# Kernel optimization log

Hardware: AMD Instinct MI355X
Metric: run time of the kernel (lower is better)

Reference implementation:

```python
import jax, jax.numpy as jnp
import numpy as np

EMBED = 1024
HEADS = 16
HEAD_DIM = EMBED // HEADS


def setup_inputs() -> dict:
    key = jax.random.key(0)
    ks = jax.random.split(key, 8)
    N, S = 4, 2048
    scale = 1.0 / np.sqrt(HEAD_DIM)
    return {
        "values": jax.random.normal(ks[0], (N, S, EMBED), jnp.float32),
        "keys": jax.random.normal(ks[1], (N, S, EMBED), jnp.float32),
        "query": jax.random.normal(ks[2], (N, S, EMBED), jnp.float32),
        "Wv": jax.random.normal(ks[3], (HEAD_DIM, HEAD_DIM), jnp.float32) * scale,
        "Wk": jax.random.normal(ks[4], (HEAD_DIM, HEAD_DIM), jnp.float32) * scale,
        "Wq": jax.random.normal(ks[5], (HEAD_DIM, HEAD_DIM), jnp.float32) * scale,
        "Wo": jax.random.normal(ks[6], (EMBED, EMBED), jnp.float32) / np.sqrt(EMBED),
        "bo": jax.random.normal(ks[7], (EMBED,), jnp.float32) * 0.01,
    }


def reference(values, keys, query, Wv, Wk, Wq, Wo, bo):
    N = query.shape[0]
    # reshape to [N, S, H, D]
    v = values.reshape(N, -1, HEADS, HEAD_DIM)
    k = keys.reshape(N, -1, HEADS, HEAD_DIM)
    q = query.reshape(N, -1, HEADS, HEAD_DIM)
    # per-head linear projections (torch Linear: x @ W.T)
    v = jnp.einsum("nshd,ed->nshe", v, Wv)
    k = jnp.einsum("nshd,ed->nshe", k, Wk)
    q = jnp.einsum("nshd,ed->nshe", q, Wq)
    # full attention matrix [N, H, Q, K]; note scale uses embed_size**0.5 as in source
    energy = jnp.einsum("nqhd,nkhd->nhqk", q, k)
    attn = jax.nn.softmax(energy / jnp.sqrt(jnp.asarray(EMBED, energy.dtype)), axis=3)
    out = jnp.einsum("nhql,nlhd->nqhd", attn, v).reshape(N, -1, EMBED)
    return out @ Wo.T + bo
```

## Files before the change

kernel.cpp:

```cpp
#include <hip/hip_runtime.h>
#include <hip/hip_bf16.h>

#define EMBED 1024
#define HEADS 16
#define HD    64
#define NB    4
#define SEQ   2048

typedef __bf16 bf16x8 __attribute__((ext_vector_type(8)));
typedef float  f32x4  __attribute__((ext_vector_type(4)));

__device__ __forceinline__ unsigned short f2bf(float f) {
    union { float f; unsigned u; } v; v.f = f;
    unsigned r = v.u + 0x7fffu + ((v.u >> 16) & 1u);
    return (unsigned short)(r >> 16);
}
__device__ __forceinline__ unsigned pack2(float a, float b) {
    return (unsigned)f2bf(a) | ((unsigned)f2bf(b) << 16);
}

__global__ __launch_bounds__(256) void cvt_kernel(const float* __restrict__ src,
                                                  unsigned short* __restrict__ dst) {
    int i = blockIdx.x * 256 + threadIdx.x;
    float4 v = ((const float4*)src)[i];
    ushort4 o;
    o.x = f2bf(v.x); o.y = f2bf(v.y); o.z = f2bf(v.z); o.w = f2bf(v.w);
    ((ushort4*)dst)[i] = o;
}

__global__ __launch_bounds__(256) void proj_kernel(
    const float* __restrict__ xq, const float* __restrict__ xk, const float* __restrict__ xv,
    const float* __restrict__ Wq, const float* __restrict__ Wk, const float* __restrict__ Wv,
    unsigned short* __restrict__ Qp, unsigned short* __restrict__ Kp, unsigned short* __restrict__ Vt)
{
    __shared__ __align__(16) unsigned short Wl[64 * 72];
    __shared__ __align__(16) unsigned short Xl[256 * 72];

    int bx = blockIdx.x;
    int p  = bx >> 9;
    int r  = bx & 511;
    int st = r & 7, h = (r >> 3) & 15, n = r >> 7;
    int s0 = st * 256;

    const float* x = (p == 0) ? xq : (p == 1) ? xk : xv;
    const float* W = (p == 0) ? Wq : (p == 1) ? Wk : Wv;
    const float sc = (p == 0) ? 0.045084220027780106f : 1.0f;

    int tid = threadIdx.x;

    for (int i = 0; i < 4; ++i) {
        int idx = tid + i * 256;
        int row = idx >> 4, c4 = idx & 15;
        float4 wv = ((const float4*)W)[row * 16 + c4];
        int o = row * 72 + c4 * 4;
        Wl[o] = f2bf(wv.x); Wl[o+1] = f2bf(wv.y); Wl[o+2] = f2bf(wv.z); Wl[o+3] = f2bf(wv.w);
    }
    const float* xbase = x + (size_t)(n * SEQ + s0) * EMBED + h * HD;
    for (int i = 0; i < 16; ++i) {
        int idx = tid + i * 256;
        int row = idx >> 4, c4 = idx & 15;
        float4 v = *(const float4*)(xbase + (size_t)row * EMBED + c4 * 4);
        int o = row * 72 + c4 * 4;
        Xl[o] = f2bf(v.x); Xl[o+1] = f2bf(v.y); Xl[o+2] = f2bf(v.z); Xl[o+3] = f2bf(v.w);
    }
    __syncthreads();

    int w = tid >> 6, lane = tid & 63, ln = lane & 15, qd = lane >> 4;

    bf16x8 a[4][2], b[4][2];
#pragma unroll
    for (int mt = 0; mt < 4; ++mt)
#pragma unroll
        for (int kt = 0; kt < 2; ++kt)
            a[mt][kt] = *(const bf16x8*)&Xl[(w * 64 + mt * 16 + ln) * 72 + kt * 32 + qd * 8];
#pragma unroll
    for (int i = 0; i < 4; ++i)
#pragma unroll
        for (int kt = 0; kt < 2; ++kt)
            b[i][kt] = *(const bf16x8*)&Wl[(i * 16 + ln) * 72 + kt * 32 + qd * 8];

    f32x4 acc[4][4];
    const f32x4 fz = {0.f, 0.f, 0.f, 0.f};
#pragma unroll
    for (int i = 0; i < 4; ++i)
#pragma unroll
        for (int j = 0; j < 4; ++j) acc[i][j] = fz;

    if (p < 2) {
#pragma unroll
        for (int i = 0; i < 4; ++i)
#pragma unroll
            for (int j = 0; j < 4; ++j) {
                acc[i][j] = __builtin_amdgcn_mfma_f32_16x16x32_bf16(b[i][0], a[j][0], acc[i][j], 0, 0, 0);
                acc[i][j] = __builtin_amdgcn_mfma_f32_16x16x32_bf16(b[i][1], a[j][1], acc[i][j], 0, 0, 0);
            }
#pragma unroll
        for (int i = 0; i < 4; ++i)
#pragma unroll
            for (int j = 0; j < 4; ++j) {
                uint2 pk;
                pk.x = pack2(acc[i][j][0] * sc, acc[i][j][1] * sc);
                pk.y = pack2(acc[i][j][2] * sc, acc[i][j][3] * sc);
                *(uint2*)&Xl[(w * 64 + j * 16 + ln) * 72 + i * 16 + qd * 4] = pk;
            }
        __syncthreads();
        unsigned short* outp = (p == 0 ? Qp : Kp) + (size_t)(n * HEADS + h) * SEQ * HD + (size_t)s0 * HD;
        for (int i = 0; i < 8; ++i) {
            int idx = tid + i * 256;
            int row = idx >> 3, ch = idx & 7;
            *(uint4*)(outp + (size_t)row * HD + ch * 8) = *(const uint4*)&Xl[row * 72 + ch * 8];
        }
    } else {
#pragma unroll
        for (int mt = 0; mt < 4; ++mt)
#pragma unroll
            for (int i = 0; i < 4; ++i) {
                acc[mt][i] = __builtin_amdgcn_mfma_f32_16x16x32_bf16(a[mt][0], b[i][0], acc[mt][i], 0, 0, 0);
                acc[mt][i] = __builtin_amdgcn_mfma_f32_16x16x32_bf16(a[mt][1], b[i][1], acc[mt][i], 0, 0, 0);
            }
        __syncthreads();
#pragma unroll
        for (int mt = 0; mt < 4; ++mt)
#pragma unroll
            for (int i = 0; i < 4; ++i) {
                uint2 pk;
                pk.x = pack2(acc[mt][i][0], acc[mt][i][1]);
                pk.y = pack2(acc[mt][i][2], acc[mt][i][3]);
                *(uint2*)&Xl[(i * 16 + ln) * 264 + w * 64 + mt * 16 + qd * 4] = pk;
            }
        __syncthreads();
        unsigned short* outp = Vt + (size_t)(n * HEADS + h) * HD * SEQ + s0;
        for (int i = 0; i < 8; ++i) {
            int idx = tid + i * 256;
            int row = idx >> 5, ch = idx & 31;
            *(uint4*)(outp + (size_t)row * SEQ + ch * 8) = *(const uint4*)&Xl[row * 264 + ch * 8];
        }
    }
}

__global__ __launch_bounds__(256, 2) void attn_kernel(
    const unsigned short* __restrict__ Qp, const unsigned short* __restrict__ Kp,
    const unsigned short* __restrict__ Vt, unsigned short* __restrict__ Xattn)
{
    __shared__ __align__(16) unsigned short Kl[2][64 * 72];
    __shared__ __align__(16) unsigned short Vl[2][64 * 72];
    __shared__ __align__(16) unsigned short Pl[256 * 72];

    int bx = blockIdx.x;
    int head = bx >> 3, qt = bx & 7;
    int n = head >> 4, h = head & 15;
    int q0 = qt * 256;

    int tid = threadIdx.x;
    int w = tid >> 6, lane = tid & 63, ln = lane & 15, qd = lane >> 4;

    const unsigned short* Qb = Qp + (size_t)head * SEQ * HD;
    const unsigned short* Kb = Kp + (size_t)head * SEQ * HD;
    const unsigned short* Vb = Vt + (size_t)head * HD * SEQ;

    bf16x8 qb[4][2];
#pragma unroll
    for (int nt = 0; nt < 4; ++nt)
#pragma unroll
        for (int kt = 0; kt < 2; ++kt)
            qb[nt][kt] = *(const bf16x8*)(Qb + (size_t)(q0 + w * 64 + nt * 16 + ln) * HD + kt * 32 + qd * 8);

    const f32x4 fz = {0.f, 0.f, 0.f, 0.f};
    f32x4 ot[4][4], l4[4];
#pragma unroll
    for (int mt = 0; mt < 4; ++mt) {
        l4[mt] = fz;
#pragma unroll
        for (int nt = 0; nt < 4; ++nt) ot[mt][nt] = fz;
    }

    bf16x8 ones;
    {
        union { short s[8]; bf16x8 v; } uo;
#pragma unroll
        for (int i = 0; i < 8; ++i) uo.s[i] = 0x3F80;
        ones = uo.v;
    }

    int srow = tid >> 3, sch = tid & 7;

    uint4 rK[2], rV[2];
#pragma unroll
    for (int i = 0; i < 2; ++i) {
        int row = srow + i * 32;
        rK[i] = *(const uint4*)(Kb + (size_t)row * HD + sch * 8);
        rV[i] = *(const uint4*)(Vb + (size_t)row * SEQ + 0 + sch * 8);
    }
#pragma unroll
    for (int i = 0; i < 2; ++i) {
        int row = srow + i * 32;
        *(uint4*)&Kl[0][row * 72 + sch * 8] = rK[i];
        *(uint4*)&Vl[0][row * 72 + sch * 8] = rV[i];
    }
#pragma unroll
    for (int i = 0; i < 2; ++i) {
        int row = srow + i * 32;
        rK[i] = *(const uint4*)(Kb + (size_t)(64 + row) * HD + sch * 8);
        rV[i] = *(const uint4*)(Vb + (size_t)row * SEQ + 64 + sch * 8);
    }

    for (int kc = 0; kc < SEQ; kc += 64) {
        int cur = (kc >> 6) & 1, nxt = cur ^ 1;
        __syncthreads();

        if (kc + 64 < SEQ) {
#pragma unroll
            for (int i = 0; i < 2; ++i) {
                int row = srow + i * 32;
                *(uint4*)&Kl[nxt][row * 72 + sch * 8] = rK[i];
                *(uint4*)&Vl[nxt][row * 72 + sch * 8] = rV[i];
            }
            int kn = kc + 128 <= SEQ - 64 ? kc + 128 : SEQ - 64;
#pragma unroll
            for (int i = 0; i < 2; ++i) {
                int row = srow + i * 32;
                rK[i] = *(const uint4*)(Kb + (size_t)(kn + row) * HD + sch * 8);
                rV[i] = *(const uint4*)(Vb + (size_t)row * SEQ + kn + sch * 8);
            }
        }

        bf16x8 kb[4][2];
#pragma unroll
        for (int mt = 0; mt < 4; ++mt)
#pragma unroll
            for (int kt = 0; kt < 2; ++kt)
                kb[mt][kt] = *(const bf16x8*)&Kl[cur][(mt * 16 + ln) * 72 + kt * 32 + qd * 8];

#pragma unroll
        for (int mh = 0; mh < 2; ++mh) {
            f32x4 st[2][4];
#pragma unroll
            for (int m2 = 0; m2 < 2; ++m2)
#pragma unroll
                for (int nt = 0; nt < 4; ++nt) {
                    int mt = mh * 2 + m2;
                    f32x4 acc = fz;
                    acc = __builtin_amdgcn_mfma_f32_16x16x32_bf16(kb[mt][0], qb[nt][0], acc, 0, 0, 0);
                    acc = __builtin_amdgcn_mfma_f32_16x16x32_bf16(kb[mt][1], qb[nt][1], acc, 0, 0, 0);
                    st[m2][nt] = acc;
                }
#pragma unroll
            for (int m2 = 0; m2 < 2; ++m2)
#pragma unroll
                for (int nt = 0; nt < 4; ++nt) {
                    int mt = mh * 2 + m2;
                    float p0 = __builtin_amdgcn_exp2f(st[m2][nt][0]);
                    float p1 = __builtin_amdgcn_exp2f(st[m2][nt][1]);
                    float p2 = __builtin_amdgcn_exp2f(st[m2][nt][2]);
                    float p3 = __builtin_amdgcn_exp2f(st[m2][nt][3]);
                    uint2 pk;
                    pk.x = pack2(p0, p1);
                    pk.y = pack2(p2, p3);
                    *(uint2*)&Pl[(w * 64 + nt * 16 + ln) * 72 + mt * 16 + qd * 4] = pk;
                }
        }
        __asm__ volatile("s_waitcnt lgkmcnt(0)" ::: "memory");

        bf16x8 pb[4][2], vf[4][2];
#pragma unroll
        for (int nt = 0; nt < 4; ++nt)
#pragma unroll
            for (int kt = 0; kt < 2; ++kt)
                pb[nt][kt] = *(const bf16x8*)&Pl[(w * 64 + nt * 16 + ln) * 72 + kt * 32 + qd * 8];
#pragma unroll
        for (int mt = 0; mt < 4; ++mt)
#pragma unroll
            for (int kt = 0; kt < 2; ++kt)
                vf[mt][kt] = *(const bf16x8*)&Vl[cur][(mt * 16 + ln) * 72 + kt * 32 + qd * 8];
#pragma unroll
        for (int nt = 0; nt < 4; ++nt) {
            l4[nt] = __builtin_amdgcn_mfma_f32_16x16x32_bf16(ones, pb[nt][0], l4[nt], 0, 0, 0);
            l4[nt] = __builtin_amdgcn_mfma_f32_16x16x32_bf16(ones, pb[nt][1], l4[nt], 0, 0, 0);
#pragma unroll
            for (int mt = 0; mt < 4; ++mt) {
                ot[mt][nt] = __builtin_amdgcn_mfma_f32_16x16x32_bf16(vf[mt][0], pb[nt][0], ot[mt][nt], 0, 0, 0);
                ot[mt][nt] = __builtin_amdgcn_mfma_f32_16x16x32_bf16(vf[mt][1], pb[nt][1], ot[mt][nt], 0, 0, 0);
            }
        }
    }

    float inv[4];
#pragma unroll
    for (int nt = 0; nt < 4; ++nt) inv[nt] = 1.0f / l4[nt][0];

#pragma unroll
    for (int mt = 0; mt < 4; ++mt)
#pragma unroll
        for (int nt = 0; nt < 4; ++nt) {
            uint2 pk;
            pk.x = pack2(ot[mt][nt][0] * inv[nt], ot[mt][nt][1] * inv[nt]);
            pk.y = pack2(ot[mt][nt][2] * inv[nt], ot[mt][nt][3] * inv[nt]);
            *(uint2*)&Pl[(w * 64 + nt * 16 + ln) * 72 + mt * 16 + qd * 4] = pk;
        }
    __syncthreads();
    unsigned short* ob = Xattn + (size_t)(n * SEQ + q0) * EMBED + h * HD;
    for (int i = 0; i < 8; ++i) {
        int idx = tid + i * 256;
        int row = idx >> 3, ch = idx & 7;
        *(uint4*)(ob + (size_t)row * EMBED + ch * 8) = *(const uint4*)&Pl[row * 72 + ch * 8];
    }
}

__global__ __launch_bounds__(256) void outproj_kernel(
    const unsigned short* __restrict__ X, const unsigned short* __restrict__ Wb,
    const float* __restrict__ bo, float* __restrict__ out)
{
    __shared__ __align__(16) unsigned short Al[128 * 72];
    __shared__ __align__(16) unsigned short Bl[128 * 72];

    int bx = blockIdx.x;
    int cm = bx >> 3, cn = bx & 7;
    int m0 = cm * 128, c0 = cn * 128;
    int tid = threadIdx.x;
    int w = tid >> 6, lane = tid & 63, ln = lane & 15, qd = lane >> 4;
    int rh = (w & 1) * 64, chh = (w >> 1) * 64;

    f32x4 acc[4][4];
    const f32x4 fz = {0.f, 0.f, 0.f, 0.f};
#pragma unroll
    for (int mt = 0; mt < 4; ++mt)
#pragma unroll
        for (int nt = 0; nt < 4; ++nt) acc[mt][nt] = fz;

    for (int k0 = 0; k0 < EMBED; k0 += 64) {
        for (int i = 0; i < 4; ++i) {
            int idx = tid + i * 256;
            int row = idx >> 3, ch = idx & 7;
            uint4 av = *(const uint4*)(X  + (size_t)(m0 + row) * EMBED + k0 + ch * 8);
            uint4 bv = *(const uint4*)(Wb + (size_t)(c0 + row) * EMBED + k0 + ch * 8);
            *(uint4*)&Al[row * 72 + ch * 8] = av;
            *(uint4*)&Bl[row * 72 + ch * 8] = bv;
        }
        __syncthreads();
        bf16x8 af[4][2], bf_[4][2];
#pragma unroll
        for (int mt = 0; mt < 4; ++mt)
#pragma unroll
            for (int kt = 0; kt < 2; ++kt)
                af[mt][kt] = *(const bf16x8*)&Al[(rh + mt * 16 + ln) * 72 + kt * 32 + qd * 8];
#pragma unroll
        for (int nt = 0; nt < 4; ++nt)
#pragma unroll
            for (int kt = 0; kt < 2; ++kt)
                bf_[nt][kt] = *(const bf16x8*)&Bl[(chh + nt * 16 + ln) * 72 + kt * 32 + qd * 8];
#pragma unroll
        for (int mt = 0; mt < 4; ++mt)
#pragma unroll
            for (int nt = 0; nt < 4; ++nt) {
                acc[mt][nt] = __builtin_amdgcn_mfma_f32_16x16x32_bf16(af[mt][0], bf_[nt][0], acc[mt][nt], 0, 0, 0);
                acc[mt][nt] = __builtin_amdgcn_mfma_f32_16x16x32_bf16(af[mt][1], bf_[nt][1], acc[mt][nt], 0, 0, 0);
            }
        __syncthreads();
    }

#pragma unroll
    for (int nt = 0; nt < 4; ++nt) {
        int col = c0 + chh + nt * 16 + ln;
        float bias = bo[col];
#pragma unroll
        for (int mt = 0; mt < 4; ++mt) {
            int row = m0 + rh + mt * 16 + qd * 4;
#pragma unroll
            for (int rg = 0; rg < 4; ++rg)
                out[(size_t)(row + rg) * EMBED + col] = acc[mt][nt][rg] + bias;
        }
    }
}

extern "C" void kernel_launch(void* const* d_in, const int* in_sizes, int n_in,
                              void* d_out, int out_size, void* d_ws, size_t ws_size,
                              hipStream_t stream) {
    const float* values = (const float*)d_in[0];
    const float* keys   = (const float*)d_in[1];
    const float* query  = (const float*)d_in[2];
    const float* Wv     = (const float*)d_in[3];
    const float* Wk     = (const float*)d_in[4];
    const float* Wq     = (const float*)d_in[5];
    const float* Wo     = (const float*)d_in[6];
    const float* bo     = (const float*)d_in[7];
    float* out = (float*)d_out;

    unsigned short* ws = (unsigned short*)d_ws;
    const size_t HSZ = (size_t)NB * HEADS * SEQ * HD;
    unsigned short* Qp = ws;
    unsigned short* Kp = Qp + HSZ;
    unsigned short* Vt = Kp + HSZ;
    unsigned short* Xa = Vt + HSZ;
    unsigned short* Wb = Xa + HSZ;

    cvt_kernel<<<1024, 256, 0, stream>>>(Wo, Wb);
    proj_kernel<<<1536, 256, 0, stream>>>(query, keys, values, Wq, Wk, Wv, Qp, Kp, Vt);
    attn_kernel<<<512, 256, 0, stream>>>(Qp, Kp, Vt, Xa);
    outproj_kernel<<<512, 256, 0, stream>>>(Xa, Wb, bo, out);
}
```

Measured before the change: 304.0 us.

## Rewrite attention with 32x32x16 MFMA and register-resident P via lane shuffles

The attention kernel moves from 16x16x32 MFMA tiles to 32x32x16 tiles with 8 waves of 32 queries each (512 threads). The exponentiated scores now stay in registers and are rearranged into the B-operand layout with cross-half-wave shuffles, so the shared-memory P buffer round trip goes away. The row sum is accumulated with scalar adds instead of extra MFMAs against a ones vector. It also raises occupancy hints and shrinks shared memory, at the cost of more shuffle and VALU work per tile.

```diff
diff --git a/kernel.cpp b/kernel.cpp
--- a/kernel.cpp
+++ b/kernel.cpp
@@ -9,6 +9,7 @@
 
 typedef __bf16 bf16x8 __attribute__((ext_vector_type(8)));
 typedef float  f32x4  __attribute__((ext_vector_type(4)));
+typedef float  f32x16 __attribute__((ext_vector_type(16)));
 
 __device__ __forceinline__ unsigned short f2bf(float f) {
     union { float f; unsigned u; } v; v.f = f;
@@ -138,171 +139,126 @@
     }
 }
 
-__global__ __launch_bounds__(256, 2) void attn_kernel(
+__global__ __launch_bounds__(512, 4) void attn_kernel(
     const unsigned short* __restrict__ Qp, const unsigned short* __restrict__ Kp,
     const unsigned short* __restrict__ Vt, unsigned short* __restrict__ Xattn)
 {
-    __shared__ __align__(16) unsigned short Kl[2][64 * 72];
-    __shared__ __align__(16) unsigned short Vl[2][64 * 72];
-    __shared__ __align__(16) unsigned short Pl[256 * 72];
+    __shared__ __align__(16) unsigned short SMEM[18432];
+    unsigned short* Kl = SMEM;
+    unsigned short* Vl = SMEM + 9216;
 
     int bx = blockIdx.x;
     int head = bx >> 3, qt = bx & 7;
-    int n = head >> 4, h = head & 15;
+    int n = head >> 4, h16 = head & 15;
     int q0 = qt * 256;
 
     int tid = threadIdx.x;
-    int w = tid >> 6, lane = tid & 63, ln = lane & 15, qd = lane >> 4;
+    int w = tid >> 6, lane = tid & 63;
+    int qc = lane & 31, hh = lane >> 5;
 
     const unsigned short* Qb = Qp + (size_t)head * SEQ * HD;
     const unsigned short* Kb = Kp + (size_t)head * SEQ * HD;
     const unsigned short* Vb = Vt + (size_t)head * HD * SEQ;
 
-    bf16x8 qb[4][2];
-#pragma unroll
-    for (int nt = 0; nt < 4; ++nt)
-#pragma unroll
-        for (int kt = 0; kt < 2; ++kt)
-            qb[nt][kt] = *(const bf16x8*)(Qb + (size_t)(q0 + w * 64 + nt * 16 + ln) * HD + kt * 32 + qd * 8);
-
-    const f32x4 fz = {0.f, 0.f, 0.f, 0.f};
-    f32x4 ot[4][4], l4[4];
-#pragma unroll
-    for (int mt = 0; mt < 4; ++mt) {
-        l4[mt] = fz;
-#pragma unroll
-        for (int nt = 0; nt < 4; ++nt) ot[mt][nt] = fz;
-    }
-
-    bf16x8 ones;
+    bf16x8 qb[4];
     {
-        union { short s[8]; bf16x8 v; } uo;
-#pragma unroll
-        for (int i = 0; i < 8; ++i) uo.s[i] = 0x3F80;
-        ones = uo.v;
-    }
+        int qrow = q0 + w * 32 + qc;
+#pragma unroll
+        for (int kk = 0; kk < 4; ++kk)
+            qb[kk] = *(const bf16x8*)(Qb + (size_t)qrow * HD + kk * 16 + hh * 8);
+    }
+
+    f32x16 ot0, ot1;
+#pragma unroll
+    for (int i = 0; i < 16; ++i) { ot0[i] = 0.f; ot1[i] = 0.f; }
+    float lsum = 0.f;
 
     int srow = tid >> 3, sch = tid & 7;
 
-    uint4 rK[2], rV[2];
-#pragma unroll
-    for (int i = 0; i < 2; ++i) {
-        int row = srow + i * 32;
-        rK[i] = *(const uint4*)(Kb + (size_t)row * HD + sch * 8);
-        rV[i] = *(const uint4*)(Vb + (size_t)row * SEQ + 0 + sch * 8);
-    }
-#pragma unroll
-    for (int i = 0; i < 2; ++i) {
-        int row = srow + i * 32;
-        *(uint4*)&Kl[0][row * 72 + sch * 8] = rK[i];
-        *(uint4*)&Vl[0][row * 72 + sch * 8] = rV[i];
-    }
-#pragma unroll
-    for (int i = 0; i < 2; ++i) {
-        int row = srow + i * 32;
-        rK[i] = *(const uint4*)(Kb + (size_t)(64 + row) * HD + sch * 8);
-        rV[i] = *(const uint4*)(Vb + (size_t)row * SEQ + 64 + sch * 8);
-    }
+    uint4 rK, rV;
+    rK = *(const uint4*)(Kb + (size_t)srow * HD + sch * 8);
+    rV = *(const uint4*)(Vb + (size_t)srow * SEQ + 0 + sch * 8);
+    *(uint4*)&Kl[srow * 72 + sch * 8] = rK;
+    *(uint4*)&Vl[srow * 72 + sch * 8] = rV;
+    rK = *(const uint4*)(Kb + (size_t)(64 + srow) * HD + sch * 8);
+    rV = *(const uint4*)(Vb + (size_t)srow * SEQ + 64 + sch * 8);
 
     for (int kc = 0; kc < SEQ; kc += 64) {
         int cur = (kc >> 6) & 1, nxt = cur ^ 1;
+        int curo = cur * 4608;
         __syncthreads();
 
         if (kc + 64 < SEQ) {
-#pragma unroll
-            for (int i = 0; i < 2; ++i) {
-                int row = srow + i * 32;
-                *(uint4*)&Kl[nxt][row * 72 + sch * 8] = rK[i];
-                *(uint4*)&Vl[nxt][row * 72 + sch * 8] = rV[i];
-            }
+            *(uint4*)&Kl[nxt * 4608 + srow * 72 + sch * 8] = rK;
+            *(uint4*)&Vl[nxt * 4608 + srow * 72 + sch * 8] = rV;
             int kn = kc + 128 <= SEQ - 64 ? kc + 128 : SEQ - 64;
-#pragma unroll
-            for (int i = 0; i < 2; ++i) {
-                int row = srow + i * 32;
-                rK[i] = *(const uint4*)(Kb + (size_t)(kn + row) * HD + sch * 8);
-                rV[i] = *(const uint4*)(Vb + (size_t)row * SEQ + kn + sch * 8);
-            }
-        }
-
-        bf16x8 kb[4][2];
-#pragma unroll
-        for (int mt = 0; mt < 4; ++mt)
-#pragma unroll
-            for (int kt = 0; kt < 2; ++kt)
-                kb[mt][kt] = *(const bf16x8*)&Kl[cur][(mt * 16 + ln) * 72 + kt * 32 + qd * 8];
-
-#pragma unroll
-        for (int mh = 0; mh < 2; ++mh) {
-            f32x4 st[2][4];
-#pragma unroll
-            for (int m2 = 0; m2 < 2; ++m2)
-#pragma unroll
-                for (int nt = 0; nt < 4; ++nt) {
-                    int mt = mh * 2 + m2;
-                    f32x4 acc = fz;
-                    acc = __builtin_amdgcn_mfma_f32_16x16x32_bf16(kb[mt][0], qb[nt][0], acc, 0, 0, 0);
-                    acc = __builtin_amdgcn_mfma_f32_16x16x32_bf16(kb[mt][1], qb[nt][1], acc, 0, 0, 0);
-                    st[m2][nt] = acc;
-                }
-#pragma unroll
-            for (int m2 = 0; m2 < 2; ++m2)
-#pragma unroll
-                for (int nt = 0; nt < 4; ++nt) {
-                    int mt = mh * 2 + m2;
-                    float p0 = __builtin_amdgcn_exp2f(st[m2][nt][0]);
-                    float p1 = __builtin_amdgcn_exp2f(st[m2][nt][1]);
-                    float p2 = __builtin_amdgcn_exp2f(st[m2][nt][2]);
-                    float p3 = __builtin_amdgcn_exp2f(st[m2][nt][3]);
-                    uint2 pk;
-                    pk.x = pack2(p0, p1);
-                    pk.y = pack2(p2, p3);
-                    *(uint2*)&Pl[(w * 64 + nt * 16 + ln) * 72 + mt * 16 + qd * 4] = pk;
-                }
-        }
-        __asm__ volatile("s_waitcnt lgkmcnt(0)" ::: "memory");
-
-        bf16x8 pb[4][2], vf[4][2];
-#pragma unroll
-        for (int nt = 0; nt < 4; ++nt)
-#pragma unroll
-            for (int kt = 0; kt < 2; ++kt)
-                pb[nt][kt] = *(const bf16x8*)&Pl[(w * 64 + nt * 16 + ln) * 72 + kt * 32 + qd * 8];
-#pragma unroll
-        for (int mt = 0; mt < 4; ++mt)
-#pragma unroll
-            for (int kt = 0; kt < 2; ++kt)
-                vf[mt][kt] = *(const bf16x8*)&Vl[cur][(mt * 16 + ln) * 72 + kt * 32 + qd * 8];
-#pragma unroll
-        for (int nt = 0; nt < 4; ++nt) {
-            l4[nt] = __builtin_amdgcn_mfma_f32_16x16x32_bf16(ones, pb[nt][0], l4[nt], 0, 0, 0);
-            l4[nt] = __builtin_amdgcn_mfma_f32_16x16x32_bf16(ones, pb[nt][1], l4[nt], 0, 0, 0);
-#pragma unroll
-            for (int mt = 0; mt < 4; ++mt) {
-                ot[mt][nt] = __builtin_amdgcn_mfma_f32_16x16x32_bf16(vf[mt][0], pb[nt][0], ot[mt][nt], 0, 0, 0);
-                ot[mt][nt] = __builtin_amdgcn_mfma_f32_16x16x32_bf16(vf[mt][1], pb[nt][1], ot[mt][nt], 0, 0, 0);
-            }
-        }
-    }
-
-    float inv[4];
-#pragma unroll
-    for (int nt = 0; nt < 4; ++nt) inv[nt] = 1.0f / l4[nt][0];
-
-#pragma unroll
-    for (int mt = 0; mt < 4; ++mt)
-#pragma unroll
-        for (int nt = 0; nt < 4; ++nt) {
-            uint2 pk;
-            pk.x = pack2(ot[mt][nt][0] * inv[nt], ot[mt][nt][1] * inv[nt]);
-            pk.y = pack2(ot[mt][nt][2] * inv[nt], ot[mt][nt][3] * inv[nt]);
-            *(uint2*)&Pl[(w * 64 + nt * 16 + ln) * 72 + mt * 16 + qd * 4] = pk;
-        }
+            rK = *(const uint4*)(Kb + (size_t)(kn + srow) * HD + sch * 8);
+            rV = *(const uint4*)(Vb + (size_t)srow * SEQ + kn + sch * 8);
+        }
+
+        unsigned pk[2][8];
+#pragma unroll
+        for (int kt = 0; kt < 2; ++kt) {
+            f32x16 c;
+#pragma unroll
+            for (int i = 0; i < 16; ++i) c[i] = 0.f;
+#pragma unroll
+            for (int kk = 0; kk < 4; ++kk) {
+                bf16x8 ka = *(const bf16x8*)&Kl[curo + (kt * 32 + qc) * 72 + kk * 16 + hh * 8];
+                c = __builtin_amdgcn_mfma_f32_32x32x16_bf16(ka, qb[kk], c, 0, 0, 0);
+            }
+#pragma unroll
+            for (int i = 0; i < 8; ++i) {
+                float p0 = __builtin_amdgcn_exp2f(c[2 * i]);
+                float p1 = __builtin_amdgcn_exp2f(c[2 * i + 1]);
+                lsum += p0 + p1;
+                pk[kt][i] = pack2(p0, p1);
+            }
+        }
+
+#pragma unroll
+        for (int g = 0; g < 4; ++g) {
+            const unsigned* P = pk[g >> 1];
+            int base = (g & 1) * 4;
+            unsigned s0 = hh ? P[base + 0] : P[base + 2];
+            unsigned s1 = hh ? P[base + 1] : P[base + 3];
+            unsigned r0 = (unsigned)__shfl_xor((int)s0, 32);
+            unsigned r1 = (unsigned)__shfl_xor((int)s1, 32);
+            union { unsigned u[4]; bf16x8 v; } bb;
+            bb.u[0] = hh ? r0 : P[base + 0];
+            bb.u[1] = hh ? r1 : P[base + 1];
+            bb.u[2] = hh ? P[base + 2] : r0;
+            bb.u[3] = hh ? P[base + 3] : r1;
+            bf16x8 va0 = *(const bf16x8*)&Vl[curo + qc * 72 + g * 16 + hh * 8];
+            bf16x8 va1 = *(const bf16x8*)&Vl[curo + (32 + qc) * 72 + g * 16 + hh * 8];
+            ot0 = __builtin_amdgcn_mfma_f32_32x32x16_bf16(va0, bb.v, ot0, 0, 0, 0);
+            ot1 = __builtin_amdgcn_mfma_f32_32x32x16_bf16(va1, bb.v, ot1, 0, 0, 0);
+        }
+    }
+
+    lsum += __shfl_xor(lsum, 32);
+    float inv = 1.0f / lsum;
+
     __syncthreads();
-    unsigned short* ob = Xattn + (size_t)(n * SEQ + q0) * EMBED + h * HD;
-    for (int i = 0; i < 8; ++i) {
-        int idx = tid + i * 256;
+    int qlocal = w * 32 + qc;
+#pragma unroll
+    for (int dt = 0; dt < 2; ++dt) {
+        const f32x16& o = dt ? ot1 : ot0;
+#pragma unroll
+        for (int g = 0; g < 4; ++g) {
+            uint2 p;
+            p.x = pack2(o[4 * g + 0] * inv, o[4 * g + 1] * inv);
+            p.y = pack2(o[4 * g + 2] * inv, o[4 * g + 3] * inv);
+            *(uint2*)&SMEM[qlocal * 72 + dt * 32 + g * 8 + hh * 4] = p;
+        }
+    }
+    __syncthreads();
+    unsigned short* ob = Xattn + (size_t)(n * SEQ + q0) * EMBED + h16 * HD;
+#pragma unroll
+    for (int i = 0; i < 4; ++i) {
+        int idx = tid + i * 512;
         int row = idx >> 3, ch = idx & 7;
-        *(uint4*)(ob + (size_t)row * EMBED + ch * 8) = *(const uint4*)&Pl[row * 72 + ch * 8];
+        *(uint4*)(ob + (size_t)row * EMBED + ch * 8) = *(const uint4*)&SMEM[row * 72 + ch * 8];
     }
 }
 
@@ -395,6 +351,6 @@
 
     cvt_kernel<<<1024, 256, 0, stream>>>(Wo, Wb);
     proj_kernel<<<1536, 256, 0, stream>>>(query, keys, values, Wq, Wk, Wv, Qp, Kp, Vt);
-    attn_kernel<<<512, 256, 0, stream>>>(Qp, Kp, Vt, Xa);
+    attn_kernel<<<512, 512, 0, stream>>>(Qp, Kp, Vt, Xa);
     outproj_kernel<<<512, 256, 0, stream>>>(Xa, Wb, bo, out);
 }
```

Result: faster. 277.8 us (-8.6%).
